# Kernel optimization log

Measured on AMD Instinct MI355X. Metric: run time of the kernel, lower is better.

## Reference

```python
import jax, jax.numpy as jnp
import numpy as np

HID = 128

def _gru_states(x, w_ih, w_hh, b_ih, b_hh):
    # x: [B,T,I]; w_ih: [3H,I]; w_hh: [3H,H]; biases: [3H]
    # Precompute input projections for all timesteps (one big GEMM).
    gi = jnp.einsum('bti,gi->tbg', x, w_ih) + b_ih  # [T,B,3H]
    B = x.shape[0]
    h0 = jnp.zeros((B, HID), dtype=x.dtype)

    def step(h, gi_t):
        gh = h @ w_hh.T + b_hh                      # [B,3H]
        i_r, i_z, i_n = jnp.split(gi_t, 3, axis=-1)
        h_r, h_z, h_n = jnp.split(gh, 3, axis=-1)
        r = jax.nn.sigmoid(i_r + h_r)
        z = jax.nn.sigmoid(i_z + h_z)
        n = jnp.tanh(i_n + r * h_n)
        h_new = (1.0 - z) * n + z * h
        return h_new, h_new

    _, states = jax.lax.scan(step, h0, gi)          # states: [T,B,H]
    return states


def setup_inputs() -> dict:
    key = jax.random.key(0)
    ks = jax.random.split(key, 7)
    B, T, I, H, E = 64, 2048, 128, HID, 64
    s_ih = 1.0 / np.sqrt(I)
    s_hh = 1.0 / np.sqrt(H)
    s_p = 1.0 / np.sqrt(H)
    return {
        'x': jax.random.normal(ks[0], (B, T, I), dtype=jnp.float32),
        'w_ih': jax.random.uniform(ks[1], (3 * H, I), jnp.float32, -s_ih, s_ih),
        'w_hh': jax.random.uniform(ks[2], (3 * H, H), jnp.float32, -s_hh, s_hh),
        'b_ih': jax.random.uniform(ks[3], (3 * H,), jnp.float32, -s_hh, s_hh),
        'b_hh': jax.random.uniform(ks[4], (3 * H,), jnp.float32, -s_hh, s_hh),
        'w_proj': jax.random.uniform(ks[5], (E, H), jnp.float32, -s_p, s_p),
        'b_proj': jax.random.uniform(ks[6], (E,), jnp.float32, -s_p, s_p),
    }


def reference(x, w_ih, w_hh, b_ih, b_hh, w_proj, b_proj):
    states = _gru_states(x, w_ih, w_hh, b_ih, b_hh)  # [T,B,H]
    pooled = states.mean(axis=0)                     # mean pooling over time -> [B,H]
    return pooled @ w_proj.T + b_proj                # [B,E]
```

## Files before the change

### kernel.cpp

```cpp
#include <hip/hip_runtime.h>
#include <math.h>

#define B_   64
#define T_   2048
#define HID_ 128
#define G3_  384
#define IN_  128
#define E_   64

#define TS_  128
#define CT_  512

typedef _Float16 f16x8 __attribute__((ext_vector_type(8)));
typedef float    f32x4 __attribute__((ext_vector_type(4)));

#define L2E  1.4426950408889634f
#define L2E2 2.8853900817779268f

#if __has_builtin(__builtin_amdgcn_exp2f)
#define EXP2(x) __builtin_amdgcn_exp2f(x)
#else
#define EXP2(x) __expf((x) * 0.6931471805599453f)
#endif

__device__ __forceinline__ float rcp_(float x) { return __builtin_amdgcn_rcpf(x); }

__device__ __forceinline__ f16x8 pack8_(float4 a, float4 b) {
    uint4 u;
    u.x = __builtin_bit_cast(unsigned, __builtin_amdgcn_cvt_pkrtz(a.x, a.y));
    u.y = __builtin_bit_cast(unsigned, __builtin_amdgcn_cvt_pkrtz(a.z, a.w));
    u.z = __builtin_bit_cast(unsigned, __builtin_amdgcn_cvt_pkrtz(b.x, b.y));
    u.w = __builtin_bit_cast(unsigned, __builtin_amdgcn_cvt_pkrtz(b.z, b.w));
    return __builtin_bit_cast(f16x8, u);
}

__device__ __forceinline__ void gemm_body(
    int g, int nTiles, int t0,
    const float* __restrict__ x, const float* __restrict__ w_ih,
    const float* __restrict__ b_ih, const float* __restrict__ b_hh,
    float* __restrict__ gi)
{
    const int tid = threadIdx.x;
    const int w   = tid >> 6;
    const int l   = tid & 63;
    const int ln  = l & 15;
    const int kq  = l >> 4;
    const int tt  = g % nTiles;
    const int b   = g / nTiles;
    const int tl_base = tt * TS_ + w * 16;

    const float* xb = x + ((size_t)b * T_ + (size_t)(t0 + tl_base)) * IN_;

    f16x8 afr[4];
    #pragma unroll
    for (int kc = 0; kc < 4; kc++) {
        const float* xr = xb + (size_t)ln * IN_ + kc * 32 + kq * 8;
        float4 p0 = *reinterpret_cast<const float4*>(xr);
        float4 p1 = *reinterpret_cast<const float4*>(xr + 4);
        afr[kc] = pack8_(p0, p1);
    }

    #pragma unroll
    for (int half = 0; half < 2; half++) {
        f32x4 acc[12];
        #pragma unroll
        for (int j = 0; j < 12; j++) acc[j] = (f32x4){0.f, 0.f, 0.f, 0.f};

        #pragma unroll
        for (int kc = 0; kc < 4; kc++) {
            #pragma unroll
            for (int j = 0; j < 12; j++) {
                const int nt = half * 12 + j;
                const float* wr = w_ih + (size_t)(nt * 16 + ln) * IN_ + kc * 32 + kq * 8;
                float4 q0 = *reinterpret_cast<const float4*>(wr);
                float4 q1 = *reinterpret_cast<const float4*>(wr + 4);
                const f16x8 bfr = pack8_(q0, q1);
                acc[j] = __builtin_amdgcn_mfma_f32_16x16x32_f16(afr[kc], bfr, acc[j], 0, 0, 0);
            }
        }

        #pragma unroll
        for (int j = 0; j < 12; j++) {
            const int col = half * 192 + j * 16 + ln;
            const float bias = b_ih[col] + (col < 256 ? b_hh[col] : 0.f);
            #pragma unroll
            for (int r = 0; r < 4; r++) {
                const size_t trow = (size_t)(tl_base + kq * 4 + r);
                gi[trow * (B_ * G3_) + (size_t)b * G3_ + col] = acc[j][r] + bias;
            }
        }
    }
}

#define REC_STEP(CUR, LD, TLOAD, PB)                                           \
  {                                                                            \
    const char* hb_ = (const char*)(&h2_sh[PB][0]) + kq * 16;                  \
    f16x8 af_[4];                                                              \
    af_[0] = __builtin_bit_cast(f16x8, *(const uint4*)(hb_));                  \
    af_[1] = __builtin_bit_cast(f16x8, *(const uint4*)(hb_ + 64));             \
    af_[2] = __builtin_bit_cast(f16x8, *(const uint4*)(hb_ + 128));            \
    af_[3] = __builtin_bit_cast(f16x8, *(const uint4*)(hb_ + 192));            \
    const float* gp_ = gib + (size_t)(TLOAD) * S;                              \
    LD[0] = gp_[cg]; LD[1] = gp_[cg + 128]; LD[2] = gp_[cg + 256];             \
    f32x4 ac_[3];                                                              \
    _Pragma("unroll")                                                          \
    for (int g = 0; g < 3; g++) ac_[g] = (f32x4){0.f, 0.f, 0.f, 0.f};          \
    _Pragma("unroll")                                                          \
    for (int kc = 0; kc < 4; kc++) {                                           \
      _Pragma("unroll")                                                        \
      for (int g = 0; g < 3; g++)                                              \
        ac_[g] = __builtin_amdgcn_mfma_f32_16x16x32_f16(af_[kc], wf[g][kc],    \
                                                        ac_[g], 0, 0, 0);      \
    }                                                                          \
    const float q_  = CUR[2] * L2E2;                                           \
    const float yr_ = fmaf(CUR[0], L2E, ac_[0][0]);                            \
    const float r_  = rcp_(1.f + EXP2(-yr_));                                  \
    const float yz_ = fmaf(CUR[1], L2E, ac_[1][0]);                            \
    const float z_  = rcp_(1.f + EXP2(-yz_));                                  \
    const float yn_ = fmaf(r_, ac_[2][0] + bh, q_);                            \
    const float u_  = rcp_(1.f + EXP2(yn_));                                   \
    const float n_  = fmaf(-2.f, u_, 1.f);                                     \
    hj = n_ + z_ * (hj - n_);                                                  \
    hs += hj;                                                                  \
    if (kq == 0) h2_sh[(PB) ^ 1][cg] = (_Float16)hj;                           \
    __syncthreads();                                                           \
  }

__device__ __forceinline__ void rec_body(
    int b,
    const float* __restrict__ gi, const float* __restrict__ w_hh,
    const float* __restrict__ b_hh,
    const float* __restrict__ w_proj, const float* __restrict__ b_proj,
    float* __restrict__ out, float* __restrict__ state,
    int t0, int t1)
{
    const int tid  = threadIdx.x;
    const int w    = tid >> 6;
    const int lane = tid & 63;
    const int ln   = lane & 15;
    const int kq   = lane >> 4;
    const int wh   = w & 3;
    const int f    = w >> 2;
    const int cg   = 16 * wh + ln + 64 * f;
    const int nT   = t1 - t0;

    __shared__ _Float16 h2_sh[2][HID_];
    __shared__ float pooled[HID_];

    f16x8 wf[3][4];
    #pragma unroll
    for (int g = 0; g < 3; g++) {
        const float s = (g == 2) ? L2E2 : L2E;
        const float* wr = w_hh + (size_t)(128 * g + cg) * HID_;
        #pragma unroll
        for (int kc = 0; kc < 4; kc++) {
            const float* p = wr + kc * 32 + kq * 8;
            float4 q0 = *reinterpret_cast<const float4*>(p);
            float4 q1 = *reinterpret_cast<const float4*>(p + 4);
            q0.x *= s; q0.y *= s; q0.z *= s; q0.w *= s;
            q1.x *= s; q1.y *= s; q1.z *= s; q1.w *= s;
            wf[g][kc] = pack8_(q0, q1);
        }
    }
    const float bh = L2E2 * b_hh[256 + cg];

    float hj, hs;
    if (t0 == 0) { hj = hs = 0.f; }
    else {
        hj = state[b * HID_ + cg];
        hs = state[B_ * HID_ + b * HID_ + cg];
    }
    if (kq == 0) h2_sh[0][cg] = (_Float16)hj;
    __syncthreads();

    const float* gib = gi + (size_t)b * G3_;
    const size_t S = (size_t)B_ * G3_;

    float g0[3], g1[3], g2[3], g3[3];
    {
        const float* p0 = gib;
        const float* p1 = gib + S;
        g0[0] = p0[cg]; g0[1] = p0[cg + 128]; g0[2] = p0[cg + 256];
        g1[0] = p1[cg]; g1[1] = p1[cg + 128]; g1[2] = p1[cg + 256];
    }

    int pb = 0;
    const int nTm1 = nT - 1;
    for (int t = 0; t < nT; t += 4) {
        int t2 = t + 2 < nTm1 ? t + 2 : nTm1;
        int t3 = t + 3 < nTm1 ? t + 3 : nTm1;
        int t4 = t + 4 < nTm1 ? t + 4 : nTm1;
        int t5 = t + 5 < nTm1 ? t + 5 : nTm1;
        REC_STEP(g0, g2, t2, pb); pb ^= 1;
        REC_STEP(g1, g3, t3, pb); pb ^= 1;
        REC_STEP(g2, g0, t4, pb); pb ^= 1;
        REC_STEP(g3, g1, t5, pb); pb ^= 1;
    }

    if (t1 < T_) {
        if (kq == 0) {
            state[b * HID_ + cg]             = hj;
            state[B_ * HID_ + b * HID_ + cg] = hs;
        }
    } else {
        if (kq == 0) pooled[cg] = hs * (1.f / (float)T_);
        __syncthreads();
        if (tid < E_) {
            const float4* wpj = reinterpret_cast<const float4*>(w_proj + (size_t)tid * HID_);
            const float4* pp  = reinterpret_cast<const float4*>(pooled);
            float a0 = 0.f, a1 = 0.f, a2 = 0.f, a3 = 0.f;
            #pragma unroll
            for (int k = 0; k < 32; k++) {
                float4 wv = wpj[k]; float4 pv = pp[k];
                a0 = fmaf(wv.x, pv.x, a0);
                a1 = fmaf(wv.y, pv.y, a1);
                a2 = fmaf(wv.z, pv.z, a2);
                a3 = fmaf(wv.w, pv.w, a3);
            }
            out[b * E_ + tid] = (a0 + a1) + (a2 + a3) + b_proj[tid];
        }
    }
}

__global__ __launch_bounds__(512, 1)
void fused(const float* __restrict__ x, const float* __restrict__ w_ih,
           const float* __restrict__ b_ih, const float* __restrict__ w_hh,
           const float* __restrict__ b_hh,
           const float* __restrict__ w_proj, const float* __restrict__ b_proj,
           const float* __restrict__ gi_rec, float* __restrict__ gi_out,
           float* __restrict__ out, float* __restrict__ state,
           int trec0, int trec1, int tg0, int nRec, int nTiles)
{
    const int bid = (int)blockIdx.x;
    if (bid < nRec) {
        rec_body(bid, gi_rec, w_hh, b_hh, w_proj, b_proj, out, state, trec0, trec1);
    } else {
        gemm_body(bid - nRec, nTiles, tg0, x, w_ih, b_ih, b_hh, gi_out);
    }
}

extern "C" void kernel_launch(void* const* d_in, const int* in_sizes, int n_in,
                              void* d_out, int out_size, void* d_ws, size_t ws_size,
                              hipStream_t stream)
{
    const float* x      = (const float*)d_in[0];
    const float* w_ih   = (const float*)d_in[1];
    const float* w_hh   = (const float*)d_in[2];
    const float* b_ih   = (const float*)d_in[3];
    const float* b_hh   = (const float*)d_in[4];
    const float* w_proj = (const float*)d_in[5];
    const float* b_proj = (const float*)d_in[6];
    float* out = (float*)d_out;

    const size_t state_bytes = (size_t)2 * B_ * HID_ * sizeof(float);
    const size_t per_t = (size_t)B_ * G3_ * sizeof(float);

    if (ws_size >= 2 * (size_t)CT_ * per_t + state_bytes) {
        float* buf[2] = { (float*)d_ws,
                          (float*)((char*)d_ws + (size_t)CT_ * per_t) };
        float* state  = (float*)((char*)d_ws + 2 * (size_t)CT_ * per_t);
        const int nTiles = CT_ / TS_;
        const int nC = T_ / CT_;
        for (int i = 0; i <= nC; i++) {
            const int rb = (i > 0)  ? B_ : 0;
            const int gb = (i < nC) ? nTiles * B_ : 0;
            fused<<<dim3(rb + gb), dim3(512), 0, stream>>>(
                x, w_ih, b_ih, w_hh, b_hh, w_proj, b_proj,
                buf[(i + 1) & 1] , buf[i & 1],
                out, state,
                (i - 1) * CT_, i * CT_, i * CT_, rb, nTiles);
        }
    } else {
        size_t avail = ws_size > state_bytes ? ws_size - state_bytes : 0;
        int cT = (int)(avail / per_t);
        if (cT > T_) cT = T_;
        cT &= ~(TS_ - 1);
        if (cT < TS_) cT = TS_;
        float* buf0  = (float*)d_ws;
        float* state = (float*)((char*)d_ws + (size_t)cT * per_t);
        for (int t0 = 0; t0 < T_; t0 += cT) {
            int t1 = t0 + cT; if (t1 > T_) t1 = T_;
            int nt = t1 - t0;
            fused<<<dim3((nt / TS_) * B_), dim3(512), 0, stream>>>(
                x, w_ih, b_ih, w_hh, b_hh, w_proj, b_proj,
                buf0, buf0, out, state, 0, 0, t0, 0, nt / TS_);
            fused<<<dim3(B_), dim3(512), 0, stream>>>(
                x, w_ih, b_ih, w_hh, b_hh, w_proj, b_proj,
                buf0, buf0, out, state, t0, t1, 0, B_, nt / TS_);
        }
    }
}
```

Baseline: 836.2 us.

## Use growing chunk sizes for GEMM/recurrence overlap and reorder gate MFMAs

Replaces the fixed 512-step chunking with chunks of increasing size (128, 256, 640, 1024), so the first GEMM chunk, which is not overlapped with the recurrence, is short. Each later chunk's input-projection GEMM runs alongside the recurrence of the previous chunk. Inside the recurrent step, the reset and candidate gate MFMAs are issued first so the reset sigmoid can be computed while the update gate MFMAs are still in flight. This shortens the serial critical path per step. The buffers are sized unevenly to match the chunk sizes, and later chunks can leave GEMM work unbalanced against the recurrence.

```diff
diff --git a/kernel.cpp b/kernel.cpp
--- a/kernel.cpp
+++ b/kernel.cpp
@@ -9,7 +9,6 @@
 #define E_   64
 
 #define TS_  128
-#define CT_  512
 
 typedef _Float16 f16x8 __attribute__((ext_vector_type(8)));
 typedef float    f32x4 __attribute__((ext_vector_type(4)));
@@ -102,24 +101,29 @@
     af_[3] = __builtin_bit_cast(f16x8, *(const uint4*)(hb_ + 192));            \
     const float* gp_ = gib + (size_t)(TLOAD) * S;                              \
     LD[0] = gp_[cg]; LD[1] = gp_[cg + 128]; LD[2] = gp_[cg + 256];             \
-    f32x4 ac_[3];                                                              \
-    _Pragma("unroll")                                                          \
-    for (int g = 0; g < 3; g++) ac_[g] = (f32x4){0.f, 0.f, 0.f, 0.f};          \
-    _Pragma("unroll")                                                          \
-    for (int kc = 0; kc < 4; kc++) {                                           \
-      _Pragma("unroll")                                                        \
-      for (int g = 0; g < 3; g++)                                              \
-        ac_[g] = __builtin_amdgcn_mfma_f32_16x16x32_f16(af_[kc], wf[g][kc],    \
-                                                        ac_[g], 0, 0, 0);      \
-    }                                                                          \
+    f32x4 a0_ = (f32x4){0.f, 0.f, 0.f, 0.f};                                   \
+    f32x4 a1_ = (f32x4){0.f, 0.f, 0.f, 0.f};                                   \
+    f32x4 a2_ = (f32x4){0.f, 0.f, 0.f, 0.f};                                   \
+    a0_ = __builtin_amdgcn_mfma_f32_16x16x32_f16(af_[0], wf[0][0], a0_, 0, 0, 0); \
+    a0_ = __builtin_amdgcn_mfma_f32_16x16x32_f16(af_[1], wf[0][1], a0_, 0, 0, 0); \
+    a0_ = __builtin_amdgcn_mfma_f32_16x16x32_f16(af_[2], wf[0][2], a0_, 0, 0, 0); \
+    a0_ = __builtin_amdgcn_mfma_f32_16x16x32_f16(af_[3], wf[0][3], a0_, 0, 0, 0); \
+    a2_ = __builtin_amdgcn_mfma_f32_16x16x32_f16(af_[0], wf[2][0], a2_, 0, 0, 0); \
+    a2_ = __builtin_amdgcn_mfma_f32_16x16x32_f16(af_[1], wf[2][1], a2_, 0, 0, 0); \
+    a2_ = __builtin_amdgcn_mfma_f32_16x16x32_f16(af_[2], wf[2][2], a2_, 0, 0, 0); \
+    a2_ = __builtin_amdgcn_mfma_f32_16x16x32_f16(af_[3], wf[2][3], a2_, 0, 0, 0); \
+    const float yr_ = fmaf(CUR[0], L2E, a0_[0]);                               \
+    const float r_  = rcp_(1.f + EXP2(-yr_));                                  \
+    a1_ = __builtin_amdgcn_mfma_f32_16x16x32_f16(af_[0], wf[1][0], a1_, 0, 0, 0); \
+    a1_ = __builtin_amdgcn_mfma_f32_16x16x32_f16(af_[1], wf[1][1], a1_, 0, 0, 0); \
+    a1_ = __builtin_amdgcn_mfma_f32_16x16x32_f16(af_[2], wf[1][2], a1_, 0, 0, 0); \
+    a1_ = __builtin_amdgcn_mfma_f32_16x16x32_f16(af_[3], wf[1][3], a1_, 0, 0, 0); \
     const float q_  = CUR[2] * L2E2;                                           \
-    const float yr_ = fmaf(CUR[0], L2E, ac_[0][0]);                            \
-    const float r_  = rcp_(1.f + EXP2(-yr_));                                  \
-    const float yz_ = fmaf(CUR[1], L2E, ac_[1][0]);                            \
-    const float z_  = rcp_(1.f + EXP2(-yz_));                                  \
-    const float yn_ = fmaf(r_, ac_[2][0] + bh, q_);                            \
+    const float yn_ = fmaf(r_, a2_[0] + bh, q_);                               \
     const float u_  = rcp_(1.f + EXP2(yn_));                                   \
     const float n_  = fmaf(-2.f, u_, 1.f);                                     \
+    const float yz_ = fmaf(CUR[1], L2E, a1_[0]);                               \
+    const float z_  = rcp_(1.f + EXP2(-yz_));                                  \
     hj = n_ + z_ * (hj - n_);                                                  \
     hs += hj;                                                                  \
     if (kq == 0) h2_sh[(PB) ^ 1][cg] = (_Float16)hj;                           \
@@ -255,20 +259,29 @@
     const size_t state_bytes = (size_t)2 * B_ * HID_ * sizeof(float);
     const size_t per_t = (size_t)B_ * G3_ * sizeof(float);
 
-    if (ws_size >= 2 * (size_t)CT_ * per_t + state_bytes) {
+    const int NCK = 4;
+    const int ck[NCK] = {128, 256, 640, 1024};
+    const size_t buf0_rows = 640, buf1_rows = 1024;
+    const size_t need = (buf0_rows + buf1_rows) * per_t + state_bytes;
+
+    if (ws_size >= need) {
         float* buf[2] = { (float*)d_ws,
-                          (float*)((char*)d_ws + (size_t)CT_ * per_t) };
-        float* state  = (float*)((char*)d_ws + 2 * (size_t)CT_ * per_t);
-        const int nTiles = CT_ / TS_;
-        const int nC = T_ / CT_;
-        for (int i = 0; i <= nC; i++) {
-            const int rb = (i > 0)  ? B_ : 0;
-            const int gb = (i < nC) ? nTiles * B_ : 0;
+                          (float*)((char*)d_ws + buf0_rows * per_t) };
+        float* state  = (float*)((char*)d_ws + (buf0_rows + buf1_rows) * per_t);
+        int st[NCK + 1];
+        st[0] = 0;
+        for (int i = 0; i < NCK; i++) st[i + 1] = st[i] + ck[i];
+        for (int i = 0; i <= NCK; i++) {
+            const int rb = (i > 0)   ? B_ : 0;
+            const int gb = (i < NCK) ? (ck[i] / TS_) * B_ : 0;
+            const int trec0 = (i > 0) ? st[i - 1] : 0;
+            const int trec1 = (i > 0) ? st[i]     : 0;
+            const int tg0   = (i < NCK) ? st[i] : 0;
+            const int nT    = (i < NCK) ? ck[i] / TS_ : 1;
             fused<<<dim3(rb + gb), dim3(512), 0, stream>>>(
                 x, w_ih, b_ih, w_hh, b_hh, w_proj, b_proj,
                 buf[(i + 1) & 1] , buf[i & 1],
-                out, state,
-                (i - 1) * CT_, i * CT_, i * CT_, rb, nTiles);
+                out, state, trec0, trec1, tg0, rb, nT);
         }
     } else {
         size_t avail = ws_size > state_bytes ? ws_size - state_bytes : 0;
```

After: 833.6 us. No clear change (-0.3%).
